# Optimization experiments

Measured on AMD Instinct MI355X. Metric: run time of the kernel, lower is better.

The kernel has to match this reference:

```python
import jax, jax.numpy as jnp
import numpy as np

N = 1_000_000     # number of cells
N_BATCHES = 64    # acquisition batches
Y_DIM = 32        # markers / embedding dim


def setup_inputs() -> dict:
    key = jax.random.key(0)
    k_b, k_w = jax.random.split(key)
    b = jax.random.randint(k_b, (N, 1), 0, N_BATCHES, dtype=jnp.int64 if jax.config.jax_enable_x64 else jnp.int32)
    weight = jax.random.normal(k_w, (N_BATCHES, Y_DIM), dtype=jnp.float32)
    return {"b": b, "weight": weight}


def reference(b, weight):
    # Original builds one-hot [N, n_batches] via scatter_, zeros row 0, then
    # matmuls with the embedding weight. That equals a direct gather
    # weight[b[:,0]] with the first sample's row forced to zero.
    effect = jnp.take(weight, b[:, 0], axis=0)          # [N, Y_DIM]
    effect = effect.at[0, :].set(0.0)                   # batch_one_hot[0,:] = 0
    return effect
```

## Files before the change

kernel.cpp:

```cpp
#include <hip/hip_runtime.h>


typedef float f32x4 __attribute__((ext_vector_type(4)));

#define WROWS 64
#define WPAD  9

__global__ __launch_bounds__(256) void batch_effect_gather_kernel(
        const int* __restrict__ b,
        const f32x4* __restrict__ w4,
        f32x4* __restrict__ out4,
        int n_cells) {
    __shared__ f32x4 sw[WROWS * WPAD];
    __shared__ int   sb[256];
    const int tid = threadIdx.x;
    const int base_cell = blockIdx.x << 8;

#pragma unroll
    for (int t = tid; t < WROWS * 8; t += 256)
        sw[(t >> 3) * WPAD + (t & 7)] = w4[t];

    int c = base_cell + tid;
    sb[tid] = (c < n_cells) ? b[c] : 0;
    __syncthreads();

    const int j         = tid & 7;
    const int lane_cell = tid >> 3;
    const int base_vec  = base_cell << 3;

    if (n_cells - base_cell >= 256) {
        f32x4 v[8];
#pragma unroll
        for (int k = 0; k < 8; ++k) {
            int cl = (k << 5) + lane_cell;
            v[k] = sw[sb[cl] * WPAD + j];
            if (base_cell + cl == 0)
                v[k] = (f32x4){0.f, 0.f, 0.f, 0.f};
        }
#pragma unroll
        for (int k = 0; k < 8; ++k)
            out4[base_vec + (k << 8) + tid] = v[k];
    } else {
        for (int k = 0; k < 8; ++k) {
            int cl = (k << 5) + lane_cell;
            if (base_cell + cl < n_cells)
                out4[base_vec + (k << 8) + tid] = sw[sb[cl] * WPAD + j];
        }
    }
}

extern "C" void kernel_launch(void* const* d_in, const int* in_sizes, int n_in,
                              void* d_out, int out_size, void* d_ws, size_t ws_size,
                              hipStream_t stream) {
    const int*   b  = (const int*)d_in[0];
    const f32x4* w4 = (const f32x4*)d_in[1];
    f32x4* out4 = (f32x4*)d_out;

    int n = in_sizes[0];
    int blocks = (n + 255) / 256;
    batch_effect_gather_kernel<<<blocks, 256, 0, stream>>>(b, w4, out4, n);
}
```

Before: 133.9 us.

## Switch gather kernel to fixed-grid grid-stride loop with per-vector index loads

Replaces the one-block-per-256-cells launch with a fixed 2048-block grid-stride loop. Each thread now handles one float4 output vector per iteration, unrolled by four, and reads the batch index straight from global memory instead of staging it in shared memory. The goal is to amortise the per-block weight-table preload over many more outputs and to cut block launch overhead. The cost is redundant index loads, since eight threads read each index, and a less regular index access pattern.

```diff
diff --git a/kernel.cpp b/kernel.cpp
--- a/kernel.cpp
+++ b/kernel.cpp
@@ -10,42 +10,38 @@
         const int* __restrict__ b,
         const f32x4* __restrict__ w4,
         f32x4* __restrict__ out4,
-        int n_cells) {
+        int n_vec) {
     __shared__ f32x4 sw[WROWS * WPAD];
-    __shared__ int   sb[256];
+
     const int tid = threadIdx.x;
-    const int base_cell = blockIdx.x << 8;
-
 #pragma unroll
     for (int t = tid; t < WROWS * 8; t += 256)
         sw[(t >> 3) * WPAD + (t & 7)] = w4[t];
-
-    int c = base_cell + tid;
-    sb[tid] = (c < n_cells) ? b[c] : 0;
     __syncthreads();
 
-    const int j         = tid & 7;
-    const int lane_cell = tid >> 3;
-    const int base_vec  = base_cell << 3;
+    const int stride = gridDim.x * 256;
+    int g = blockIdx.x * 256 + tid;
 
-    if (n_cells - base_cell >= 256) {
-        f32x4 v[8];
-#pragma unroll
-        for (int k = 0; k < 8; ++k) {
-            int cl = (k << 5) + lane_cell;
-            v[k] = sw[sb[cl] * WPAD + j];
-            if (base_cell + cl == 0)
-                v[k] = (f32x4){0.f, 0.f, 0.f, 0.f};
-        }
-#pragma unroll
-        for (int k = 0; k < 8; ++k)
-            out4[base_vec + (k << 8) + tid] = v[k];
-    } else {
-        for (int k = 0; k < 8; ++k) {
-            int cl = (k << 5) + lane_cell;
-            if (base_cell + cl < n_cells)
-                out4[base_vec + (k << 8) + tid] = sw[sb[cl] * WPAD + j];
-        }
+    for (; g + 3 * stride < n_vec; g += 4 * stride) {
+        const int c0 = g, c1 = g + stride, c2 = g + 2 * stride, c3 = g + 3 * stride;
+        const int b0 = b[c0 >> 3];
+        const int b1 = b[c1 >> 3];
+        const int b2 = b[c2 >> 3];
+        const int b3 = b[c3 >> 3];
+        f32x4 v0 = sw[b0 * WPAD + (c0 & 7)];
+        f32x4 v1 = sw[b1 * WPAD + (c1 & 7)];
+        f32x4 v2 = sw[b2 * WPAD + (c2 & 7)];
+        f32x4 v3 = sw[b3 * WPAD + (c3 & 7)];
+        if (c0 < 8) v0 = (f32x4){0.f, 0.f, 0.f, 0.f};
+        out4[c0] = v0;
+        out4[c1] = v1;
+        out4[c2] = v2;
+        out4[c3] = v3;
+    }
+    for (; g < n_vec; g += stride) {
+        f32x4 v = sw[b[g >> 3] * WPAD + (g & 7)];
+        if (g < 8) v = (f32x4){0.f, 0.f, 0.f, 0.f};
+        out4[g] = v;
     }
 }
 
@@ -56,7 +52,7 @@
     const f32x4* w4 = (const f32x4*)d_in[1];
     f32x4* out4 = (f32x4*)d_out;
 
-    int n = in_sizes[0];
-    int blocks = (n + 255) / 256;
-    batch_effect_gather_kernel<<<blocks, 256, 0, stream>>>(b, w4, out4, n);
+    int n_vec = in_sizes[0] * 8;
+    int blocks = 2048;
+    batch_effect_gather_kernel<<<blocks, 256, 0, stream>>>(b, w4, out4, n_vec);
 }
```

Measured after the change: 135.1 us. Within noise of the previous version (+0.9%).
